# Optimization experiments

Hardware: AMD Instinct MI355X
Metric: run time of the kernel (lower is better)

Reference implementation:

```python
import jax, jax.numpy as jnp
import numpy as np

B, N, R, E = 4, 50000, 100000, 1_600_000   # batch, nodes (wavelets_col), wavelets_row, nnz
D_IN, H1, H2, D_OUT = 32, 32, 16, 1
NEG_SLOPE = 0.2


def _xavier(k, shape):
    lim = float(np.sqrt(6.0 / (shape[0] + shape[1])))
    return jax.random.uniform(k, shape, jnp.float32, -lim, lim)


def setup_inputs() -> dict:
    key = jax.random.key(0)
    ks = jax.random.split(key, 16)
    # wavelets: sparse (R x N); inverse wavelets: sparse (N x R)
    w_rows = jax.random.randint(ks[0], (E,), 0, R)
    w_cols = jax.random.randint(ks[1], (E,), 0, N)
    wi_rows = jax.random.randint(ks[2], (E,), 0, N)
    wi_cols = jax.random.randint(ks[3], (E,), 0, R)
    return {
        "wavelets_indices": jnp.stack([w_rows, w_cols]),
        "wavelets_values": jax.random.normal(ks[4], (E,), jnp.float32) * 0.05,
        "wavelets_inverse_indices": jnp.stack([wi_rows, wi_cols]),
        "wavelets_inverse_values": jax.random.normal(ks[5], (E,), jnp.float32) * 0.05,
        "x_features": jax.random.normal(ks[6], (B, N, D_IN), jnp.float32),
        "W1": _xavier(ks[7], (D_IN, H1)),
        "diag1": 0.9 + 0.2 * jax.random.uniform(ks[8], (R,), jnp.float32),
        "W2": _xavier(ks[9], (H1, H2)),
        "diag2": 0.9 + 0.2 * jax.random.uniform(ks[10], (R,), jnp.float32),
        "reg_co_w": _xavier(ks[11], (H2, D_OUT)),
        "reg_co_b": jnp.zeros((D_OUT,), jnp.float32),
        "reg_co2_w": _xavier(ks[12], (H2, D_OUT)),
        "reg_co2_b": jnp.zeros((D_OUT,), jnp.float32),
    }


def _gw_layer(x, W, diag, w_idx, w_val, wi_idx, wi_val):
    # filtered = X @ W  -> (B, N, d)
    h = jnp.einsum("bnd,de->bne", x, W)
    d = W.shape[1]
    # T = wavelets (R x N) @ h  : scatter-add of gathered edge messages
    msg = h[:, w_idx[1], :] * w_val[None, :, None]          # (B, E, d)
    t = jnp.zeros((x.shape[0], R, d), h.dtype).at[:, w_idx[0], :].add(msg)
    # out = (wavelets_inverse * diag) (N x R) @ T  (diag rescales columns)
    coef = wi_val * diag[wi_idx[1]]                         # (E,)
    msg2 = t[:, wi_idx[1], :] * coef[None, :, None]         # (B, E, d)
    out = jnp.zeros((x.shape[0], N, d), h.dtype).at[:, wi_idx[0], :].add(msg2)
    return jax.nn.leaky_relu(out, NEG_SLOPE)                # dropout p=0.0 -> identity


def reference(wavelets_indices, wavelets_values, wavelets_inverse_indices,
              wavelets_inverse_values, x_features, W1, diag1, W2, diag2,
              reg_co_w, reg_co_b, reg_co2_w, reg_co2_b):
    x = _gw_layer(x_features, W1, diag1, wavelets_indices, wavelets_values,
                  wavelets_inverse_indices, wavelets_inverse_values)
    x = _gw_layer(x, W2, diag2, wavelets_indices, wavelets_values,
                  wavelets_inverse_indices, wavelets_inverse_values)
    co = x[:, -2, :] @ reg_co_w + reg_co_b                  # (B, 1)
    co2 = x[:, -1, :] @ reg_co2_w + reg_co2_b               # (B, 1)
    return jnp.concatenate([co[:, None, :], co2[:, None, :]], axis=1)  # (B, 2, 1)
```

## Files before the change

kernel.cpp:

```cpp
#include <hip/hip_runtime.h>

#define NEG_SLOPE 0.2f

static const int B = 4, N = 50000, R = 100000, E = 1600000;
static const int X2_CAP = 4096;
static const int R2_CAP = 4096;
static const int N1_CAP = 4096;
static const int RS_CAP = 49152;
static const int WDEG  = 64;
static const int WIDEG = 96;
static const int RBW = 3200;
static const int NBW = 1600;
static const int ZWORDS = RS_CAP + N1_CAP + RBW + NBW + 8;

__global__ void scanA(const int4* __restrict__ wi_rows4, const int4* __restrict__ wi_cols4,
                      const float4* __restrict__ wi_val4,
                      unsigned* __restrict__ bitsRS, int* __restrict__ rslot,
                      int* __restrict__ slotrow, int2* __restrict__ x2list,
                      int* __restrict__ tails, int e4) {
    int i = blockIdx.x * blockDim.x + threadIdx.x;
    if (i >= e4) return;
    int4 r = wi_rows4[i];
    int rr[4] = {r.x, r.y, r.z, r.w};
    bool any = false;
#pragma unroll
    for (int j = 0; j < 4; ++j) any = any || (rr[j] >= N - 2);
    if (!any) return;
    int4 c = wi_cols4[i];
    float4 v = wi_val4[i];
    int cc[4] = {c.x, c.y, c.z, c.w};
    float vv[4] = {v.x, v.y, v.z, v.w};
#pragma unroll
    for (int j = 0; j < 4; ++j) {
        if (rr[j] >= N - 2) {
            int col = cc[j];
            unsigned m = 1u << (col & 31);
            unsigned old = atomicOr(&bitsRS[col >> 5], m);
            if (!(old & m)) {
                int s = atomicAdd(&tails[3], 1);
                if (s < RS_CAP) { rslot[col] = s; slotrow[s] = col; }
            }
            int q = atomicAdd(&tails[0], 1);
            if (q < X2_CAP)
                x2list[q] = make_int2(col * 2 + (rr[j] - (N - 2)),
                                      __float_as_int(vv[j]));
        }
    }
}

__global__ void scanB(const int4* __restrict__ w_rows4, const int4* __restrict__ w_cols4,
                      const unsigned* __restrict__ bitsRS, unsigned* __restrict__ bitsN1,
                      int* __restrict__ n1slot, int* __restrict__ tails, int e4) {
    __shared__ int lcount, gbase;
    __shared__ int buf[1024];
    if (threadIdx.x == 0) {
        lcount = 0;
        if (blockIdx.x == 0) tails[4] = tails[3];
    }
    __syncthreads();
    int lane = threadIdx.x & 63;
    int i = blockIdx.x * blockDim.x + threadIdx.x;
    int4 r = make_int4(-1, -1, -1, -1);
    if (i < e4) r = w_rows4[i];
    int rr[4] = {r.x, r.y, r.z, r.w};
    unsigned fb[4];
#pragma unroll
    for (int j = 0; j < 4; ++j)
        fb[j] = (rr[j] >= 0) ? ((bitsRS[rr[j] >> 5] >> (rr[j] & 31)) & 1u) : 0u;
    bool anyf = (fb[0] | fb[1] | fb[2] | fb[3]) != 0u;
    int4 c = make_int4(0, 0, 0, 0);
    if (anyf) c = w_cols4[i];
    int cc[4] = {c.x, c.y, c.z, c.w};
#pragma unroll
    for (int j = 0; j < 4; ++j) {
        bool isnew = false;
        int n = 0;
        if (fb[j]) {
            n = cc[j];
            unsigned m = 1u << (n & 31);
            unsigned old = atomicOr(&bitsN1[n >> 5], m);
            isnew = (old & m) == 0u;
        }
        unsigned long long mb = __ballot(isnew);
        if (mb) {
            int leader = __ffsll(mb) - 1;
            int b0 = 0;
            if (lane == leader) b0 = atomicAdd(&lcount, __popcll(mb));
            b0 = __shfl(b0, leader);
            if (isnew) {
                int p = b0 + __popcll(mb & ((1ull << lane) - 1));
                if (p < 1024) buf[p] = n;
            }
        }
    }
    __syncthreads();
    int lc = lcount; if (lc > 1024) lc = 1024;
    if (threadIdx.x == 0) gbase = atomicAdd(&tails[2], lc);
    __syncthreads();
    for (int t = threadIdx.x; t < lc; t += blockDim.x) {
        int slot = gbase + t;
        if (slot < N1_CAP) n1slot[buf[t]] = slot;
    }
}

__global__ void scanC(const int4* __restrict__ wi_rows4, const int4* __restrict__ wi_cols4,
                      const float4* __restrict__ wi_val4, const float* __restrict__ diag1,
                      const unsigned* __restrict__ bitsN1, const int* __restrict__ n1slot,
                      unsigned* __restrict__ bitsRS, int* __restrict__ rslot,
                      int* __restrict__ slotrow, int* __restrict__ wi_cntC,
                      int2* __restrict__ wi_pairs, int* __restrict__ tails, int e4) {
    __shared__ int lcount, gbase;
    __shared__ int buf[1024];
    if (threadIdx.x == 0) lcount = 0;
    __syncthreads();
    int lane = threadIdx.x & 63;
    int i = blockIdx.x * blockDim.x + threadIdx.x;
    int4 r = make_int4(-1, -1, -1, -1);
    if (i < e4) r = wi_rows4[i];
    int rr[4] = {r.x, r.y, r.z, r.w};
    unsigned fb[4];
#pragma unroll
    for (int j = 0; j < 4; ++j)
        fb[j] = (rr[j] >= 0) ? ((bitsN1[rr[j] >> 5] >> (rr[j] & 31)) & 1u) : 0u;
    bool anyf = (fb[0] | fb[1] | fb[2] | fb[3]) != 0u;
    int4 c = make_int4(0, 0, 0, 0);
    float4 v = make_float4(0.f, 0.f, 0.f, 0.f);
    if (anyf) { c = wi_cols4[i]; v = wi_val4[i]; }
    int cc[4] = {c.x, c.y, c.z, c.w};
    float vv[4] = {v.x, v.y, v.z, v.w};
#pragma unroll
    for (int j = 0; j < 4; ++j) {
        bool isnew = false;
        int col = 0;
        if (fb[j]) {
            col = cc[j];
            float cf = vv[j] * diag1[col];
            int slot = n1slot[rr[j]];
            if (slot >= 0 && slot < N1_CAP) {
                int pos = atomicAdd(&wi_cntC[slot], 1);
                if (pos < WIDEG)
                    wi_pairs[(size_t)slot * WIDEG + pos] =
                        make_int2(col, __float_as_int(cf));
            }
            unsigned m = 1u << (col & 31);
            unsigned old = atomicOr(&bitsRS[col >> 5], m);
            isnew = (old & m) == 0u;
        }
        unsigned long long mb = __ballot(isnew);
        if (mb) {
            int leader = __ffsll(mb) - 1;
            int b0 = 0;
            if (lane == leader) b0 = atomicAdd(&lcount, __popcll(mb));
            b0 = __shfl(b0, leader);
            if (isnew) {
                int p = b0 + __popcll(mb & ((1ull << lane) - 1));
                if (p < 1024) buf[p] = col;
            }
        }
    }
    __syncthreads();
    int lc = lcount; if (lc > 1024) lc = 1024;
    if (threadIdx.x == 0) gbase = atomicAdd(&tails[3], lc);
    __syncthreads();
    for (int t = threadIdx.x; t < lc; t += blockDim.x) {
        int col = buf[t];
        int s = gbase + t;
        if (s < RS_CAP) { rslot[col] = s; slotrow[s] = col; }
    }
}

__global__ void scanD(const int4* __restrict__ w_rows4, const int4* __restrict__ w_cols4,
                      const float4* __restrict__ w_val4,
                      const unsigned* __restrict__ bitsRS, const int* __restrict__ rslot,
                      int* __restrict__ w_cntC, int2* __restrict__ w_pairs, int e4) {
    int i = blockIdx.x * blockDim.x + threadIdx.x;
    if (i >= e4) return;
    int4 r = w_rows4[i];
    int rr[4] = {r.x, r.y, r.z, r.w};
    unsigned fb[4];
#pragma unroll
    for (int j = 0; j < 4; ++j) fb[j] = (bitsRS[rr[j] >> 5] >> (rr[j] & 31)) & 1u;
    if (!(fb[0] | fb[1] | fb[2] | fb[3])) return;
    int4 c = w_cols4[i];
    float4 v = w_val4[i];
    int cc[4] = {c.x, c.y, c.z, c.w};
    float vv[4] = {v.x, v.y, v.z, v.w};
    int s[4];
#pragma unroll
    for (int j = 0; j < 4; ++j) s[j] = fb[j] ? rslot[rr[j]] : RS_CAP;
#pragma unroll
    for (int j = 0; j < 4; ++j) {
        if (fb[j] && s[j] < RS_CAP) {
            int pos = atomicAdd(&w_cntC[s[j]], 1);
            if (pos < WDEG)
                w_pairs[(size_t)s[j] * WDEG + pos] =
                    make_int2(cc[j], __float_as_int(vv[j]));
        }
    }
}

__global__ void gather_t1(const float* __restrict__ x, float* __restrict__ t1C,
                          const int* __restrict__ w_cntC, const int2* __restrict__ w_pairs,
                          const int* __restrict__ tails) {
    int tot = tails[3]; if (tot > RS_CAP) tot = RS_CAP;
    int total = tot * 32;
    int gstride = gridDim.x * blockDim.x;
    for (int idx = blockIdx.x * blockDim.x + threadIdx.x; idx < total; idx += gstride) {
        int s = idx >> 5;
        int rem = idx & 31;
        int c4 = rem & 7;
        int b = rem >> 3;
        int L = w_cntC[s]; if (L > WDEG) L = WDEG;
        const int2* pr = w_pairs + (size_t)s * WDEG;
        const float4* sb = (const float4*)x + (size_t)b * N * 8 + c4;
        float4 acc = make_float4(0.f, 0.f, 0.f, 0.f);
        int i = 0;
        int L4 = L & ~3;
        for (; i < L4; i += 4) {
            int2 p0 = pr[i + 0];
            int2 p1 = pr[i + 1];
            int2 p2 = pr[i + 2];
            int2 p3 = pr[i + 3];
            float4 s0 = sb[(size_t)p0.x * 8];
            float4 s1 = sb[(size_t)p1.x * 8];
            float4 s2 = sb[(size_t)p2.x * 8];
            float4 s3 = sb[(size_t)p3.x * 8];
            float v0 = __int_as_float(p0.y), v1 = __int_as_float(p1.y);
            float v2 = __int_as_float(p2.y), v3 = __int_as_float(p3.y);
            acc.x += v0 * s0.x + v1 * s1.x + v2 * s2.x + v3 * s3.x;
            acc.y += v0 * s0.y + v1 * s1.y + v2 * s2.y + v3 * s3.y;
            acc.z += v0 * s0.z + v1 * s1.z + v2 * s2.z + v3 * s3.z;
            acc.w += v0 * s0.w + v1 * s1.w + v2 * s2.w + v3 * s3.w;
        }
        for (; i < L; ++i) {
            int2 p = pr[i];
            float4 sv = sb[(size_t)p.x * 8];
            float v = __int_as_float(p.y);
            acc.x += v * sv.x; acc.y += v * sv.y; acc.z += v * sv.z; acc.w += v * sv.w;
        }
        ((float4*)t1C)[(size_t)s * 32 + b * 8 + c4] = acc;
    }
}

__global__ void __launch_bounds__(256) x1mlp(
        const float* __restrict__ W1, const float* __restrict__ W2,
        const int* __restrict__ tails,
        const int* __restrict__ wi_cntC, const int2* __restrict__ wi_pairs,
        const int* __restrict__ rslot, const float* __restrict__ t1C,
        float* __restrict__ h2C) {
    __shared__ float W1s[1024], W2s[512];
    __shared__ float uls[8][128];
    __shared__ float ufin[128], x1ls[128];
    for (int i = threadIdx.x; i < 1024; i += 256) W1s[i] = W1[i];
    for (int i = threadIdx.x; i < 512; i += 256) W2s[i] = W2[i];
    int n1c = tails[2]; if (n1c > N1_CAP) n1c = N1_CAP;
    int g = threadIdx.x >> 5, t32 = threadIdx.x & 31;
    int b = t32 >> 3, c4 = t32 & 7;
    const float4* t1f4 = (const float4*)t1C;
    for (int s = blockIdx.x; s < n1c; s += gridDim.x) {
        int L = wi_cntC[s]; if (L > WIDEG) L = WIDEG;
        const int2* wip = wi_pairs + (size_t)s * WIDEG;
        float4 acc = make_float4(0.f, 0.f, 0.f, 0.f);
        for (int e = g; e < L; e += 8) {
            int2 pe = wip[e];
            int rs = rslot[pe.x];
            float coef = __int_as_float(pe.y);
            if (rs < RS_CAP) {
                float4 tv = t1f4[(size_t)rs * 32 + b * 8 + c4];
                acc.x += coef * tv.x; acc.y += coef * tv.y;
                acc.z += coef * tv.z; acc.w += coef * tv.w;
            }
        }
        float* up = &uls[g][b * 32 + c4 * 4];
        up[0] = acc.x; up[1] = acc.y; up[2] = acc.z; up[3] = acc.w;
        __syncthreads();
        if (threadIdx.x < 128) {
            float sum = 0.f;
#pragma unroll
            for (int gg = 0; gg < 8; ++gg) sum += uls[gg][threadIdx.x];
            ufin[threadIdx.x] = sum;
        }
        __syncthreads();
        if (threadIdx.x < 128) {
            int bb = threadIdx.x >> 5, c = threadIdx.x & 31;
            const float* ur = &ufin[bb * 32];
            float o = 0.f;
#pragma unroll
            for (int k = 0; k < 32; ++k) o += ur[k] * W1s[k * 32 + c];
            x1ls[threadIdx.x] = o > 0.f ? o : NEG_SLOPE * o;
        }
        __syncthreads();
        if (threadIdx.x < 64) {
            int bb = threadIdx.x >> 4, c = threadIdx.x & 15;
            const float* xr = &x1ls[bb * 32];
            float o = 0.f;
#pragma unroll
            for (int k = 0; k < 32; ++k) o += xr[k] * W2s[k * 16 + c];
            h2C[(size_t)s * 64 + bb * 16 + c] = o;
        }
        __syncthreads();
    }
}

__global__ void t2x2heads(const float* __restrict__ h2C,
                          const int* __restrict__ w_cntC, const int2* __restrict__ w_pairs,
                          const int* __restrict__ n1slot, const int* __restrict__ rslot,
                          const int* __restrict__ tails, float* __restrict__ t2C,
                          const int2* __restrict__ x2list,
                          const float* __restrict__ diag2,
                          const float* __restrict__ rw1, const float* __restrict__ rb1,
                          const float* __restrict__ rw2, const float* __restrict__ rb2,
                          float* __restrict__ out) {
    int r2c = tails[4]; if (r2c > R2_CAP) r2c = R2_CAP;
    for (int idx = threadIdx.x; idx < r2c * 16; idx += blockDim.x) {
        int s = idx >> 4;
        int rem = idx & 15;
        int c4 = rem & 3;
        int b = rem >> 2;
        int L = w_cntC[s]; if (L > WDEG) L = WDEG;
        const int2* pr = w_pairs + (size_t)s * WDEG;
        const float4* sb = (const float4*)h2C + b * 4 + c4;
        float4 acc = make_float4(0.f, 0.f, 0.f, 0.f);
        for (int i = 0; i < L; ++i) {
            int2 p = pr[i];
            int hs = n1slot[p.x];
            float v = __int_as_float(p.y);
            if (hs >= 0 && hs < N1_CAP) {
                float4 sv = sb[(size_t)hs * 16];
                acc.x += v * sv.x; acc.y += v * sv.y; acc.z += v * sv.z; acc.w += v * sv.w;
            }
        }
        ((float4*)t2C)[(size_t)s * 16 + b * 4 + c4] = acc;
    }
    __syncthreads();

    int cnt = tails[0]; if (cnt > X2_CAP) cnt = X2_CAP;
    int g = threadIdx.x >> 6, l = threadIdx.x & 63;
    int b = l >> 4, c = l & 15;
    float a0 = 0.f, a1 = 0.f;
    for (int i = g; i < cnt; i += 16) {
        int2 rec = x2list[i];
        int col = rec.x >> 1;
        int s = rslot[col];
        float coef = __int_as_float(rec.y) * diag2[col];
        float v = (s < R2_CAP) ? t2C[(size_t)s * 64 + b * 16 + c] * coef : 0.f;
        if (rec.x & 1) a1 += v; else a0 += v;
    }
    __shared__ float red0[16][64], red1[16][64], xs[2][64];
    red0[g][l] = a0; red1[g][l] = a1;
    __syncthreads();
    if (threadIdx.x < 64) {
        float s0 = 0.f, s1 = 0.f;
#pragma unroll
        for (int gg = 0; gg < 16; ++gg) { s0 += red0[gg][threadIdx.x]; s1 += red1[gg][threadIdx.x]; }
        xs[0][threadIdx.x] = s0; xs[1][threadIdx.x] = s1;
    }
    __syncthreads();
    if (threadIdx.x < 8) {
        int bb = threadIdx.x >> 1, which = threadIdx.x & 1;
        const float* w = which ? rw2 : rw1;
        float acc = which ? rb2[0] : rb1[0];
        for (int k = 0; k < 16; ++k) {
            float xv = xs[which][bb * 16 + k];
            xv = xv > 0.f ? xv : NEG_SLOPE * xv;
            acc += xv * w[k];
        }
        out[bb * 2 + which] = acc;
    }
}

extern "C" void kernel_launch(void* const* d_in, const int* in_sizes, int n_in,
                              void* d_out, int out_size, void* d_ws, size_t ws_size,
                              hipStream_t stream) {
    const int*   w_rows  = (const int*)d_in[0];
    const int*   w_cols  = ((const int*)d_in[0]) + E;
    const float* w_val   = (const float*)d_in[1];
    const int*   wi_rows = (const int*)d_in[2];
    const int*   wi_cols = ((const int*)d_in[2]) + E;
    const float* wi_val  = (const float*)d_in[3];
    const float* x       = (const float*)d_in[4];
    const float* W1      = (const float*)d_in[5];
    const float* diag1   = (const float*)d_in[6];
    const float* W2      = (const float*)d_in[7];
    const float* diag2   = (const float*)d_in[8];
    const float* rw1     = (const float*)d_in[9];
    const float* rb1     = (const float*)d_in[10];
    const float* rw2     = (const float*)d_in[11];
    const float* rb2     = (const float*)d_in[12];
    float* out = (float*)d_out;

    float* t1C = (float*)d_ws;
    float* h2C = t1C + (size_t)RS_CAP * 128;
    float* t2C = h2C + (size_t)N1_CAP * 64;
    int* ip = (int*)(t2C + (size_t)R2_CAP * 64);
    int* w_cntC  = ip; ip += RS_CAP;
    int* wi_cntC = ip; ip += N1_CAP;
    unsigned* bitsRS = (unsigned*)ip; ip += RBW;
    unsigned* bitsN1 = (unsigned*)ip; ip += NBW;
    int* tails = ip; ip += 8;
    int* rslot   = ip; ip += R;
    int* slotrow = ip; ip += RS_CAP;
    int* n1slot  = ip; ip += N;
    int2* x2list = (int2*)ip; ip += 2 * X2_CAP;
    int2* w_pairs  = (int2*)ip; ip += 2 * (size_t)RS_CAP * WDEG;
    int2* wi_pairs = (int2*)ip; ip += 2 * (size_t)N1_CAP * WIDEG;

    const int e4 = E / 4;
    const int blk = 256;
    const int scanGrid = (e4 + blk - 1) / blk;

    (void)hipMemsetAsync(w_cntC, 0, (size_t)ZWORDS * sizeof(int), stream);

    scanA<<<scanGrid, blk, 0, stream>>>((const int4*)wi_rows, (const int4*)wi_cols,
                                        (const float4*)wi_val, bitsRS, rslot, slotrow,
                                        x2list, tails, e4);
    scanB<<<scanGrid, blk, 0, stream>>>((const int4*)w_rows, (const int4*)w_cols,
                                        bitsRS, bitsN1, n1slot, tails, e4);
    scanC<<<scanGrid, blk, 0, stream>>>((const int4*)wi_rows, (const int4*)wi_cols,
                                        (const float4*)wi_val, diag1, bitsN1, n1slot,
                                        bitsRS, rslot, slotrow, wi_cntC, wi_pairs,
                                        tails, e4);
    scanD<<<scanGrid, blk, 0, stream>>>((const int4*)w_rows, (const int4*)w_cols,
                                        (const float4*)w_val, bitsRS, rslot,
                                        w_cntC, w_pairs, e4);
    gather_t1<<<2048, blk, 0, stream>>>(x, t1C, w_cntC, w_pairs, tails);
    x1mlp<<<1024, blk, 0, stream>>>(W1, W2, tails, wi_cntC, wi_pairs,
                                    rslot, t1C, h2C);
    t2x2heads<<<1, 1024, 0, stream>>>(h2C, w_cntC, w_pairs, n1slot, rslot, tails,
                                      t2C, x2list, diag2, rw1, rb1, rw2, rb2, out);
}
```

Baseline: 272.2 us.

## Replace padded wavelet buckets with CSR and fuse T1 gather into x1mlp

The fixed-degree (WDEG) per-row buckets of wavelet edges are replaced by a compact CSR layout. It is built by a count pass, a single-block prefix scan and a placement pass. The separate gather_t1 kernel and its t1C intermediate buffer are removed: x1mlp now computes each needed T1 row on the fly from the CSR edges and x while it accumulates the inverse-wavelet edges. The change is meant to cut the write and re-read of the large t1C buffer and the padded pair storage, and to drop the unused slotrow writes. In exchange it adds one more full scan over the edge list, a serial single-block prefix kernel, and possible repeated recomputation of shared T1 rows inside x1mlp.

```diff
diff --git a/kernel.cpp b/kernel.cpp
--- a/kernel.cpp
+++ b/kernel.cpp
@@ -7,7 +7,6 @@
 static const int R2_CAP = 4096;
 static const int N1_CAP = 4096;
 static const int RS_CAP = 49152;
-static const int WDEG  = 64;
 static const int WIDEG = 96;
 static const int RBW = 3200;
 static const int NBW = 1600;
@@ -16,8 +15,7 @@
 __global__ void scanA(const int4* __restrict__ wi_rows4, const int4* __restrict__ wi_cols4,
                       const float4* __restrict__ wi_val4,
                       unsigned* __restrict__ bitsRS, int* __restrict__ rslot,
-                      int* __restrict__ slotrow, int2* __restrict__ x2list,
-                      int* __restrict__ tails, int e4) {
+                      int2* __restrict__ x2list, int* __restrict__ tails, int e4) {
     int i = blockIdx.x * blockDim.x + threadIdx.x;
     if (i >= e4) return;
     int4 r = wi_rows4[i];
@@ -38,7 +36,7 @@
             unsigned old = atomicOr(&bitsRS[col >> 5], m);
             if (!(old & m)) {
                 int s = atomicAdd(&tails[3], 1);
-                if (s < RS_CAP) { rslot[col] = s; slotrow[s] = col; }
+                if (s < RS_CAP) rslot[col] = s;
             }
             int q = atomicAdd(&tails[0], 1);
             if (q < X2_CAP)
@@ -95,7 +93,7 @@
     }
     __syncthreads();
     int lc = lcount; if (lc > 1024) lc = 1024;
-    if (threadIdx.x == 0) gbase = atomicAdd(&tails[2], lc);
+    if (threadIdx.x == 0 && lc > 0) gbase = atomicAdd(&tails[2], lc);
     __syncthreads();
     for (int t = threadIdx.x; t < lc; t += blockDim.x) {
         int slot = gbase + t;
@@ -107,8 +105,8 @@
                       const float4* __restrict__ wi_val4, const float* __restrict__ diag1,
                       const unsigned* __restrict__ bitsN1, const int* __restrict__ n1slot,
                       unsigned* __restrict__ bitsRS, int* __restrict__ rslot,
-                      int* __restrict__ slotrow, int* __restrict__ wi_cntC,
-                      int2* __restrict__ wi_pairs, int* __restrict__ tails, int e4) {
+                      int* __restrict__ wi_cntC, int2* __restrict__ wi_pairs,
+                      int* __restrict__ tails, int e4) {
     __shared__ int lcount, gbase;
     __shared__ int buf[1024];
     if (threadIdx.x == 0) lcount = 0;
@@ -160,19 +158,63 @@
     }
     __syncthreads();
     int lc = lcount; if (lc > 1024) lc = 1024;
-    if (threadIdx.x == 0) gbase = atomicAdd(&tails[3], lc);
+    if (threadIdx.x == 0 && lc > 0) gbase = atomicAdd(&tails[3], lc);
     __syncthreads();
     for (int t = threadIdx.x; t < lc; t += blockDim.x) {
-        int col = buf[t];
         int s = gbase + t;
-        if (s < RS_CAP) { rslot[col] = s; slotrow[s] = col; }
-    }
-}
-
-__global__ void scanD(const int4* __restrict__ w_rows4, const int4* __restrict__ w_cols4,
-                      const float4* __restrict__ w_val4,
-                      const unsigned* __restrict__ bitsRS, const int* __restrict__ rslot,
-                      int* __restrict__ w_cntC, int2* __restrict__ w_pairs, int e4) {
+        if (s < RS_CAP) rslot[buf[t]] = s;
+    }
+}
+
+__global__ void countD(const int4* __restrict__ w_rows4,
+                       const unsigned* __restrict__ bitsRS, const int* __restrict__ rslot,
+                       int* __restrict__ w_cnt, int e4) {
+    int i = blockIdx.x * blockDim.x + threadIdx.x;
+    if (i >= e4) return;
+    int4 r = w_rows4[i];
+    int rr[4] = {r.x, r.y, r.z, r.w};
+    unsigned fb[4];
+#pragma unroll
+    for (int j = 0; j < 4; ++j) fb[j] = (bitsRS[rr[j] >> 5] >> (rr[j] & 31)) & 1u;
+    if (!(fb[0] | fb[1] | fb[2] | fb[3])) return;
+#pragma unroll
+    for (int j = 0; j < 4; ++j) {
+        if (fb[j]) {
+            int s = rslot[rr[j]];
+            if (s >= 0 && s < RS_CAP) atomicAdd(&w_cnt[s], 1);
+        }
+    }
+}
+
+__global__ void prefixD(const int* __restrict__ w_cnt, int* __restrict__ rowptr,
+                        int* __restrict__ cursor, const int* __restrict__ tails) {
+    __shared__ int ssum[1024];
+    int tot = tails[3]; if (tot > RS_CAP) tot = RS_CAP;
+    int per = (tot + 1023) >> 10;
+    int lo = threadIdx.x * per;
+    int hi = lo + per; if (hi > tot) hi = tot;
+    int s = 0;
+    for (int i = lo; i < hi; ++i) s += w_cnt[i];
+    ssum[threadIdx.x] = s;
+    __syncthreads();
+    for (int off = 1; off < 1024; off <<= 1) {
+        int t = (threadIdx.x >= off) ? ssum[threadIdx.x - off] : 0;
+        __syncthreads();
+        ssum[threadIdx.x] += t;
+        __syncthreads();
+    }
+    int run = ssum[threadIdx.x] - s;
+    for (int i = lo; i < hi; ++i) {
+        rowptr[i] = run;
+        cursor[i] = run;
+        run += w_cnt[i];
+    }
+}
+
+__global__ void placeD(const int4* __restrict__ w_rows4, const int4* __restrict__ w_cols4,
+                       const float4* __restrict__ w_val4,
+                       const unsigned* __restrict__ bitsRS, const int* __restrict__ rslot,
+                       int* __restrict__ cursor, int2* __restrict__ w_pairs, int e4) {
     int i = blockIdx.x * blockDim.x + threadIdx.x;
     if (i >= e4) return;
     int4 r = w_rows4[i];
@@ -190,63 +232,19 @@
     for (int j = 0; j < 4; ++j) s[j] = fb[j] ? rslot[rr[j]] : RS_CAP;
 #pragma unroll
     for (int j = 0; j < 4; ++j) {
-        if (fb[j] && s[j] < RS_CAP) {
-            int pos = atomicAdd(&w_cntC[s[j]], 1);
-            if (pos < WDEG)
-                w_pairs[(size_t)s[j] * WDEG + pos] =
-                    make_int2(cc[j], __float_as_int(vv[j]));
-        }
-    }
-}
-
-__global__ void gather_t1(const float* __restrict__ x, float* __restrict__ t1C,
-                          const int* __restrict__ w_cntC, const int2* __restrict__ w_pairs,
-                          const int* __restrict__ tails) {
-    int tot = tails[3]; if (tot > RS_CAP) tot = RS_CAP;
-    int total = tot * 32;
-    int gstride = gridDim.x * blockDim.x;
-    for (int idx = blockIdx.x * blockDim.x + threadIdx.x; idx < total; idx += gstride) {
-        int s = idx >> 5;
-        int rem = idx & 31;
-        int c4 = rem & 7;
-        int b = rem >> 3;
-        int L = w_cntC[s]; if (L > WDEG) L = WDEG;
-        const int2* pr = w_pairs + (size_t)s * WDEG;
-        const float4* sb = (const float4*)x + (size_t)b * N * 8 + c4;
-        float4 acc = make_float4(0.f, 0.f, 0.f, 0.f);
-        int i = 0;
-        int L4 = L & ~3;
-        for (; i < L4; i += 4) {
-            int2 p0 = pr[i + 0];
-            int2 p1 = pr[i + 1];
-            int2 p2 = pr[i + 2];
-            int2 p3 = pr[i + 3];
-            float4 s0 = sb[(size_t)p0.x * 8];
-            float4 s1 = sb[(size_t)p1.x * 8];
-            float4 s2 = sb[(size_t)p2.x * 8];
-            float4 s3 = sb[(size_t)p3.x * 8];
-            float v0 = __int_as_float(p0.y), v1 = __int_as_float(p1.y);
-            float v2 = __int_as_float(p2.y), v3 = __int_as_float(p3.y);
-            acc.x += v0 * s0.x + v1 * s1.x + v2 * s2.x + v3 * s3.x;
-            acc.y += v0 * s0.y + v1 * s1.y + v2 * s2.y + v3 * s3.y;
-            acc.z += v0 * s0.z + v1 * s1.z + v2 * s2.z + v3 * s3.z;
-            acc.w += v0 * s0.w + v1 * s1.w + v2 * s2.w + v3 * s3.w;
-        }
-        for (; i < L; ++i) {
-            int2 p = pr[i];
-            float4 sv = sb[(size_t)p.x * 8];
-            float v = __int_as_float(p.y);
-            acc.x += v * sv.x; acc.y += v * sv.y; acc.z += v * sv.z; acc.w += v * sv.w;
-        }
-        ((float4*)t1C)[(size_t)s * 32 + b * 8 + c4] = acc;
+        if (fb[j] && s[j] >= 0 && s[j] < RS_CAP) {
+            int pos = atomicAdd(&cursor[s[j]], 1);
+            w_pairs[pos] = make_int2(cc[j], __float_as_int(vv[j]));
+        }
     }
 }
 
 __global__ void __launch_bounds__(256) x1mlp(
-        const float* __restrict__ W1, const float* __restrict__ W2,
-        const int* __restrict__ tails,
+        const float* __restrict__ x, const float* __restrict__ W1,
+        const float* __restrict__ W2, const int* __restrict__ tails,
         const int* __restrict__ wi_cntC, const int2* __restrict__ wi_pairs,
-        const int* __restrict__ rslot, const float* __restrict__ t1C,
+        const int* __restrict__ rslot, const int* __restrict__ rowptr,
+        const int* __restrict__ w_cnt, const int2* __restrict__ w_pairs,
         float* __restrict__ h2C) {
     __shared__ float W1s[1024], W2s[512];
     __shared__ float uls[8][128];
@@ -256,7 +254,7 @@
     int n1c = tails[2]; if (n1c > N1_CAP) n1c = N1_CAP;
     int g = threadIdx.x >> 5, t32 = threadIdx.x & 31;
     int b = t32 >> 3, c4 = t32 & 7;
-    const float4* t1f4 = (const float4*)t1C;
+    const float4* xb = (const float4*)x + (size_t)b * N * 8 + c4;
     for (int s = blockIdx.x; s < n1c; s += gridDim.x) {
         int L = wi_cntC[s]; if (L > WIDEG) L = WIDEG;
         const int2* wip = wi_pairs + (size_t)s * WIDEG;
@@ -265,11 +263,37 @@
             int2 pe = wip[e];
             int rs = rslot[pe.x];
             float coef = __int_as_float(pe.y);
-            if (rs < RS_CAP) {
-                float4 tv = t1f4[(size_t)rs * 32 + b * 8 + c4];
-                acc.x += coef * tv.x; acc.y += coef * tv.y;
-                acc.z += coef * tv.z; acc.w += coef * tv.w;
-            }
+            if (rs < 0 || rs >= RS_CAP) continue;
+            int start = rowptr[rs];
+            int Lw = w_cnt[rs];
+            const int2* pr = w_pairs + start;
+            float4 t = make_float4(0.f, 0.f, 0.f, 0.f);
+            int i = 0;
+            int L4 = Lw & ~3;
+            for (; i < L4; i += 4) {
+                int2 p0 = pr[i + 0];
+                int2 p1 = pr[i + 1];
+                int2 p2 = pr[i + 2];
+                int2 p3 = pr[i + 3];
+                float4 s0 = xb[(size_t)p0.x * 8];
+                float4 s1 = xb[(size_t)p1.x * 8];
+                float4 s2 = xb[(size_t)p2.x * 8];
+                float4 s3 = xb[(size_t)p3.x * 8];
+                float v0 = __int_as_float(p0.y), v1 = __int_as_float(p1.y);
+                float v2 = __int_as_float(p2.y), v3 = __int_as_float(p3.y);
+                t.x += v0 * s0.x + v1 * s1.x + v2 * s2.x + v3 * s3.x;
+                t.y += v0 * s0.y + v1 * s1.y + v2 * s2.y + v3 * s3.y;
+                t.z += v0 * s0.z + v1 * s1.z + v2 * s2.z + v3 * s3.z;
+                t.w += v0 * s0.w + v1 * s1.w + v2 * s2.w + v3 * s3.w;
+            }
+            for (; i < Lw; ++i) {
+                int2 p = pr[i];
+                float4 sv = xb[(size_t)p.x * 8];
+                float v = __int_as_float(p.y);
+                t.x += v * sv.x; t.y += v * sv.y; t.z += v * sv.z; t.w += v * sv.w;
+            }
+            acc.x += coef * t.x; acc.y += coef * t.y;
+            acc.z += coef * t.z; acc.w += coef * t.w;
         }
         float* up = &uls[g][b * 32 + c4 * 4];
         up[0] = acc.x; up[1] = acc.y; up[2] = acc.z; up[3] = acc.w;
@@ -303,7 +327,8 @@
 }
 
 __global__ void t2x2heads(const float* __restrict__ h2C,
-                          const int* __restrict__ w_cntC, const int2* __restrict__ w_pairs,
+                          const int* __restrict__ rowptr, const int* __restrict__ w_cnt,
+                          const int2* __restrict__ w_pairs,
                           const int* __restrict__ n1slot, const int* __restrict__ rslot,
                           const int* __restrict__ tails, float* __restrict__ t2C,
                           const int2* __restrict__ x2list,
@@ -317,8 +342,8 @@
         int rem = idx & 15;
         int c4 = rem & 3;
         int b = rem >> 2;
-        int L = w_cntC[s]; if (L > WDEG) L = WDEG;
-        const int2* pr = w_pairs + (size_t)s * WDEG;
+        int L = w_cnt[s];
+        const int2* pr = w_pairs + rowptr[s];
         const float4* sb = (const float4*)h2C + b * 4 + c4;
         float4 acc = make_float4(0.f, 0.f, 0.f, 0.f);
         for (int i = 0; i < L; ++i) {
@@ -343,7 +368,7 @@
         int col = rec.x >> 1;
         int s = rslot[col];
         float coef = __int_as_float(rec.y) * diag2[col];
-        float v = (s < R2_CAP) ? t2C[(size_t)s * 64 + b * 16 + c] * coef : 0.f;
+        float v = (s >= 0 && s < R2_CAP) ? t2C[(size_t)s * 64 + b * 16 + c] * coef : 0.f;
         if (rec.x & 1) a1 += v; else a0 += v;
     }
     __shared__ float red0[16][64], red1[16][64], xs[2][64];
@@ -389,43 +414,44 @@
     const float* rb2     = (const float*)d_in[12];
     float* out = (float*)d_out;
 
-    float* t1C = (float*)d_ws;
-    float* h2C = t1C + (size_t)RS_CAP * 128;
+    float* h2C = (float*)d_ws;
     float* t2C = h2C + (size_t)N1_CAP * 64;
     int* ip = (int*)(t2C + (size_t)R2_CAP * 64);
-    int* w_cntC  = ip; ip += RS_CAP;
+    int* w_cnt   = ip; ip += RS_CAP;
     int* wi_cntC = ip; ip += N1_CAP;
     unsigned* bitsRS = (unsigned*)ip; ip += RBW;
     unsigned* bitsN1 = (unsigned*)ip; ip += NBW;
     int* tails = ip; ip += 8;
-    int* rslot   = ip; ip += R;
-    int* slotrow = ip; ip += RS_CAP;
-    int* n1slot  = ip; ip += N;
+    int* rowptr = ip; ip += RS_CAP + 8;
+    int* cursor = ip; ip += RS_CAP;
+    int* rslot  = ip; ip += R;
+    int* n1slot = ip; ip += N;
     int2* x2list = (int2*)ip; ip += 2 * X2_CAP;
-    int2* w_pairs  = (int2*)ip; ip += 2 * (size_t)RS_CAP * WDEG;
+    int2* w_pairs  = (int2*)ip; ip += 2 * (size_t)E;
     int2* wi_pairs = (int2*)ip; ip += 2 * (size_t)N1_CAP * WIDEG;
 
     const int e4 = E / 4;
     const int blk = 256;
     const int scanGrid = (e4 + blk - 1) / blk;
 
-    (void)hipMemsetAsync(w_cntC, 0, (size_t)ZWORDS * sizeof(int), stream);
+    (void)hipMemsetAsync(w_cnt, 0, (size_t)ZWORDS * sizeof(int), stream);
 
     scanA<<<scanGrid, blk, 0, stream>>>((const int4*)wi_rows, (const int4*)wi_cols,
-                                        (const float4*)wi_val, bitsRS, rslot, slotrow,
+                                        (const float4*)wi_val, bitsRS, rslot,
                                         x2list, tails, e4);
     scanB<<<scanGrid, blk, 0, stream>>>((const int4*)w_rows, (const int4*)w_cols,
                                         bitsRS, bitsN1, n1slot, tails, e4);
     scanC<<<scanGrid, blk, 0, stream>>>((const int4*)wi_rows, (const int4*)wi_cols,
                                         (const float4*)wi_val, diag1, bitsN1, n1slot,
-                                        bitsRS, rslot, slotrow, wi_cntC, wi_pairs,
-                                        tails, e4);
-    scanD<<<scanGrid, blk, 0, stream>>>((const int4*)w_rows, (const int4*)w_cols,
-                                        (const float4*)w_val, bitsRS, rslot,
-                                        w_cntC, w_pairs, e4);
-    gather_t1<<<2048, blk, 0, stream>>>(x, t1C, w_cntC, w_pairs, tails);
-    x1mlp<<<1024, blk, 0, stream>>>(W1, W2, tails, wi_cntC, wi_pairs,
-                                    rslot, t1C, h2C);
-    t2x2heads<<<1, 1024, 0, stream>>>(h2C, w_cntC, w_pairs, n1slot, rslot, tails,
-                                      t2C, x2list, diag2, rw1, rb1, rw2, rb2, out);
-}
+                                        bitsRS, rslot, wi_cntC, wi_pairs, tails, e4);
+    countD<<<scanGrid, blk, 0, stream>>>((const int4*)w_rows, bitsRS, rslot, w_cnt, e4);
+    prefixD<<<1, 1024, 0, stream>>>(w_cnt, rowptr, cursor, tails);
+    placeD<<<scanGrid, blk, 0, stream>>>((const int4*)w_rows, (const int4*)w_cols,
+                                         (const float4*)w_val, bitsRS, rslot,
+                                         cursor, w_pairs, e4);
+    x1mlp<<<1024, blk, 0, stream>>>(x, W1, W2, tails, wi_cntC, wi_pairs,
+                                    rslot, rowptr, w_cnt, w_pairs, h2C);
+    t2x2heads<<<1, 1024, 0, stream>>>(h2C, rowptr, w_cnt, w_pairs, n1slot, rslot,
+                                      tails, t2C, x2list, diag2,
+                                      rw1, rb1, rw2, rb2, out);
+}
```

New measurement: 360.3 us. 1.32x slower.

## Fuse final t2/heads kernel into x1mlp via last-block completion counter

Applied to the files above, without the earlier changes.

Removes the separate single-block t2x2heads launch and runs its work in the last-finishing block of x1mlp, detected with a threadfence and an atomic counter in tails[5]. This saves one kernel launch and its scheduling gap, but the tail work now runs on a 256-thread block instead of 1024 threads, so that serial phase has less parallelism. It also drops the unused slotrow array and its writes, skips the atomicAdd in blocks that found nothing new, and adds bounds checks against negative slot values.

```diff
diff --git a/kernel.cpp b/kernel.cpp
--- a/kernel.cpp
+++ b/kernel.cpp
@@ -16,8 +16,7 @@
 __global__ void scanA(const int4* __restrict__ wi_rows4, const int4* __restrict__ wi_cols4,
                       const float4* __restrict__ wi_val4,
                       unsigned* __restrict__ bitsRS, int* __restrict__ rslot,
-                      int* __restrict__ slotrow, int2* __restrict__ x2list,
-                      int* __restrict__ tails, int e4) {
+                      int2* __restrict__ x2list, int* __restrict__ tails, int e4) {
     int i = blockIdx.x * blockDim.x + threadIdx.x;
     if (i >= e4) return;
     int4 r = wi_rows4[i];
@@ -38,7 +37,7 @@
             unsigned old = atomicOr(&bitsRS[col >> 5], m);
             if (!(old & m)) {
                 int s = atomicAdd(&tails[3], 1);
-                if (s < RS_CAP) { rslot[col] = s; slotrow[s] = col; }
+                if (s < RS_CAP) rslot[col] = s;
             }
             int q = atomicAdd(&tails[0], 1);
             if (q < X2_CAP)
@@ -95,7 +94,7 @@
     }
     __syncthreads();
     int lc = lcount; if (lc > 1024) lc = 1024;
-    if (threadIdx.x == 0) gbase = atomicAdd(&tails[2], lc);
+    if (threadIdx.x == 0 && lc > 0) gbase = atomicAdd(&tails[2], lc);
     __syncthreads();
     for (int t = threadIdx.x; t < lc; t += blockDim.x) {
         int slot = gbase + t;
@@ -107,8 +106,8 @@
                       const float4* __restrict__ wi_val4, const float* __restrict__ diag1,
                       const unsigned* __restrict__ bitsN1, const int* __restrict__ n1slot,
                       unsigned* __restrict__ bitsRS, int* __restrict__ rslot,
-                      int* __restrict__ slotrow, int* __restrict__ wi_cntC,
-                      int2* __restrict__ wi_pairs, int* __restrict__ tails, int e4) {
+                      int* __restrict__ wi_cntC, int2* __restrict__ wi_pairs,
+                      int* __restrict__ tails, int e4) {
     __shared__ int lcount, gbase;
     __shared__ int buf[1024];
     if (threadIdx.x == 0) lcount = 0;
@@ -160,12 +159,11 @@
     }
     __syncthreads();
     int lc = lcount; if (lc > 1024) lc = 1024;
-    if (threadIdx.x == 0) gbase = atomicAdd(&tails[3], lc);
+    if (threadIdx.x == 0 && lc > 0) gbase = atomicAdd(&tails[3], lc);
     __syncthreads();
     for (int t = threadIdx.x; t < lc; t += blockDim.x) {
-        int col = buf[t];
         int s = gbase + t;
-        if (s < RS_CAP) { rslot[col] = s; slotrow[s] = col; }
+        if (s < RS_CAP) rslot[buf[t]] = s;
     }
 }
 
@@ -190,7 +188,7 @@
     for (int j = 0; j < 4; ++j) s[j] = fb[j] ? rslot[rr[j]] : RS_CAP;
 #pragma unroll
     for (int j = 0; j < 4; ++j) {
-        if (fb[j] && s[j] < RS_CAP) {
+        if (fb[j] && s[j] >= 0 && s[j] < RS_CAP) {
             int pos = atomicAdd(&w_cntC[s[j]], 1);
             if (pos < WDEG)
                 w_pairs[(size_t)s[j] * WDEG + pos] =
@@ -244,13 +242,20 @@
 
 __global__ void __launch_bounds__(256) x1mlp(
         const float* __restrict__ W1, const float* __restrict__ W2,
-        const int* __restrict__ tails,
+        int* __restrict__ tails,
         const int* __restrict__ wi_cntC, const int2* __restrict__ wi_pairs,
         const int* __restrict__ rslot, const float* __restrict__ t1C,
-        float* __restrict__ h2C) {
+        float* __restrict__ h2C,
+        const int* __restrict__ w_cntC, const int2* __restrict__ w_pairs,
+        const int* __restrict__ n1slot, float* __restrict__ t2C,
+        const int2* __restrict__ x2list, const float* __restrict__ diag2,
+        const float* __restrict__ rw1, const float* __restrict__ rb1,
+        const float* __restrict__ rw2, const float* __restrict__ rb2,
+        float* __restrict__ out) {
     __shared__ float W1s[1024], W2s[512];
     __shared__ float uls[8][128];
     __shared__ float ufin[128], x1ls[128];
+    __shared__ int isLast;
     for (int i = threadIdx.x; i < 1024; i += 256) W1s[i] = W1[i];
     for (int i = threadIdx.x; i < 512; i += 256) W2s[i] = W2[i];
     int n1c = tails[2]; if (n1c > N1_CAP) n1c = N1_CAP;
@@ -265,7 +270,7 @@
             int2 pe = wip[e];
             int rs = rslot[pe.x];
             float coef = __int_as_float(pe.y);
-            if (rs < RS_CAP) {
+            if (rs >= 0 && rs < RS_CAP) {
                 float4 tv = t1f4[(size_t)rs * 32 + b * 8 + c4];
                 acc.x += coef * tv.x; acc.y += coef * tv.y;
                 acc.z += coef * tv.z; acc.w += coef * tv.w;
@@ -300,26 +305,26 @@
         }
         __syncthreads();
     }
-}
-
-__global__ void t2x2heads(const float* __restrict__ h2C,
-                          const int* __restrict__ w_cntC, const int2* __restrict__ w_pairs,
-                          const int* __restrict__ n1slot, const int* __restrict__ rslot,
-                          const int* __restrict__ tails, float* __restrict__ t2C,
-                          const int2* __restrict__ x2list,
-                          const float* __restrict__ diag2,
-                          const float* __restrict__ rw1, const float* __restrict__ rb1,
-                          const float* __restrict__ rw2, const float* __restrict__ rb2,
-                          float* __restrict__ out) {
+
+    __threadfence();
+    if (threadIdx.x == 0) {
+        int old = atomicAdd(&tails[5], 1);
+        isLast = (old == (int)gridDim.x - 1);
+    }
+    __syncthreads();
+    if (!isLast) return;
+    __threadfence();
+
+    __shared__ float red0[4][64], red1[4][64], xs[2][64];
     int r2c = tails[4]; if (r2c > R2_CAP) r2c = R2_CAP;
-    for (int idx = threadIdx.x; idx < r2c * 16; idx += blockDim.x) {
+    for (int idx = threadIdx.x; idx < r2c * 16; idx += 256) {
         int s = idx >> 4;
         int rem = idx & 15;
-        int c4 = rem & 3;
-        int b = rem >> 2;
+        int cc4 = rem & 3;
+        int bb = rem >> 2;
         int L = w_cntC[s]; if (L > WDEG) L = WDEG;
         const int2* pr = w_pairs + (size_t)s * WDEG;
-        const float4* sb = (const float4*)h2C + b * 4 + c4;
+        const float4* sb = (const float4*)h2C + bb * 4 + cc4;
         float4 acc = make_float4(0.f, 0.f, 0.f, 0.f);
         for (int i = 0; i < L; ++i) {
             int2 p = pr[i];
@@ -330,42 +335,41 @@
                 acc.x += v * sv.x; acc.y += v * sv.y; acc.z += v * sv.z; acc.w += v * sv.w;
             }
         }
-        ((float4*)t2C)[(size_t)s * 16 + b * 4 + c4] = acc;
+        ((float4*)t2C)[(size_t)s * 16 + bb * 4 + cc4] = acc;
     }
     __syncthreads();
 
     int cnt = tails[0]; if (cnt > X2_CAP) cnt = X2_CAP;
-    int g = threadIdx.x >> 6, l = threadIdx.x & 63;
-    int b = l >> 4, c = l & 15;
+    int g2 = threadIdx.x >> 6, l = threadIdx.x & 63;
+    int bb = l >> 4, cix = l & 15;
     float a0 = 0.f, a1 = 0.f;
-    for (int i = g; i < cnt; i += 16) {
+    for (int i = g2; i < cnt; i += 4) {
         int2 rec = x2list[i];
         int col = rec.x >> 1;
         int s = rslot[col];
         float coef = __int_as_float(rec.y) * diag2[col];
-        float v = (s < R2_CAP) ? t2C[(size_t)s * 64 + b * 16 + c] * coef : 0.f;
+        float v = (s >= 0 && s < R2_CAP) ? t2C[(size_t)s * 64 + bb * 16 + cix] * coef : 0.f;
         if (rec.x & 1) a1 += v; else a0 += v;
     }
-    __shared__ float red0[16][64], red1[16][64], xs[2][64];
-    red0[g][l] = a0; red1[g][l] = a1;
+    red0[g2][l] = a0; red1[g2][l] = a1;
     __syncthreads();
     if (threadIdx.x < 64) {
         float s0 = 0.f, s1 = 0.f;
 #pragma unroll
-        for (int gg = 0; gg < 16; ++gg) { s0 += red0[gg][threadIdx.x]; s1 += red1[gg][threadIdx.x]; }
+        for (int gg = 0; gg < 4; ++gg) { s0 += red0[gg][threadIdx.x]; s1 += red1[gg][threadIdx.x]; }
         xs[0][threadIdx.x] = s0; xs[1][threadIdx.x] = s1;
     }
     __syncthreads();
     if (threadIdx.x < 8) {
-        int bb = threadIdx.x >> 1, which = threadIdx.x & 1;
+        int bo = threadIdx.x >> 1, which = threadIdx.x & 1;
         const float* w = which ? rw2 : rw1;
         float acc = which ? rb2[0] : rb1[0];
         for (int k = 0; k < 16; ++k) {
-            float xv = xs[which][bb * 16 + k];
+            float xv = xs[which][bo * 16 + k];
             xv = xv > 0.f ? xv : NEG_SLOPE * xv;
             acc += xv * w[k];
         }
-        out[bb * 2 + which] = acc;
+        out[bo * 2 + which] = acc;
     }
 }
 
@@ -398,9 +402,8 @@
     unsigned* bitsRS = (unsigned*)ip; ip += RBW;
     unsigned* bitsN1 = (unsigned*)ip; ip += NBW;
     int* tails = ip; ip += 8;
-    int* rslot   = ip; ip += R;
-    int* slotrow = ip; ip += RS_CAP;
-    int* n1slot  = ip; ip += N;
+    int* rslot  = ip; ip += R;
+    int* n1slot = ip; ip += N;
     int2* x2list = (int2*)ip; ip += 2 * X2_CAP;
     int2* w_pairs  = (int2*)ip; ip += 2 * (size_t)RS_CAP * WDEG;
     int2* wi_pairs = (int2*)ip; ip += 2 * (size_t)N1_CAP * WIDEG;
@@ -412,20 +415,18 @@
     (void)hipMemsetAsync(w_cntC, 0, (size_t)ZWORDS * sizeof(int), stream);
 
     scanA<<<scanGrid, blk, 0, stream>>>((const int4*)wi_rows, (const int4*)wi_cols,
-                                        (const float4*)wi_val, bitsRS, rslot, slotrow,
+                                        (const float4*)wi_val, bitsRS, rslot,
                                         x2list, tails, e4);
     scanB<<<scanGrid, blk, 0, stream>>>((const int4*)w_rows, (const int4*)w_cols,
                                         bitsRS, bitsN1, n1slot, tails, e4);
     scanC<<<scanGrid, blk, 0, stream>>>((const int4*)wi_rows, (const int4*)wi_cols,
                                         (const float4*)wi_val, diag1, bitsN1, n1slot,
-                                        bitsRS, rslot, slotrow, wi_cntC, wi_pairs,
-                                        tails, e4);
+                                        bitsRS, rslot, wi_cntC, wi_pairs, tails, e4);
     scanD<<<scanGrid, blk, 0, stream>>>((const int4*)w_rows, (const int4*)w_cols,
                                         (const float4*)w_val, bitsRS, rslot,
                                         w_cntC, w_pairs, e4);
     gather_t1<<<2048, blk, 0, stream>>>(x, t1C, w_cntC, w_pairs, tails);
-    x1mlp<<<1024, blk, 0, stream>>>(W1, W2, tails, wi_cntC, wi_pairs,
-                                    rslot, t1C, h2C);
-    t2x2heads<<<1, 1024, 0, stream>>>(h2C, w_cntC, w_pairs, n1slot, rslot, tails,
-                                      t2C, x2list, diag2, rw1, rb1, rw2, rb2, out);
-}
+    x1mlp<<<1024, blk, 0, stream>>>(W1, W2, tails, wi_cntC, wi_pairs, rslot, t1C, h2C,
+                                    w_cntC, w_pairs, n1slot, t2C, x2list, diag2,
+                                    rw1, rb1, rw2, rb2, out);
+}
```

Result: slower. 385.2 us (+41.5%).
